# Optimization experiments

Measured on AMD Instinct MI355X. Metric: run time of the kernel, lower is better.

Reference implementation:

```python
import jax, jax.numpy as jnp
import numpy as np

EPS = 1e-20

def _conv(x, w, pad):
    return jax.lax.conv_general_dilated(
        x, w, (1, 1), [(pad, pad), (pad, pad)],
        dimension_numbers=('NCHW', 'OIHW', 'NCHW'))

def _nconv(x, c, w_raw, b, pad):
    # Normalized convolution with SoftPlus-enforced positive weights.
    w = jax.nn.softplus(w_raw)
    denom = _conv(c, w, pad)
    nomin = _conv(x * c, w, pad)
    out = nomin / (denom + EPS) + b[None, :, None, None]
    s = jnp.sum(w.reshape(w.shape[0], -1), axis=-1)  # per-out-channel kernel sum
    cout = denom / s[None, :, None, None]
    return out, cout

def _pool_gather(x, c):
    # max_pool2d(c, 2, 2, return_indices=True), then gather x at those indices.
    B, C, H, W = c.shape
    win = lambda t: t.reshape(B, C, H // 2, 2, W // 2, 2).transpose(0, 1, 2, 4, 3, 5).reshape(B, C, H // 2, W // 2, 4)
    cw, xw = win(c), win(x)
    idx = jnp.argmax(cw, axis=-1)
    take = lambda t: jnp.take_along_axis(t, idx[..., None], axis=-1)[..., 0]
    return take(xw), take(cw) / 4.0  # c1_ds /= 4

def _up2(t):
    return jnp.repeat(jnp.repeat(t, 2, axis=2), 2, axis=3)

def setup_inputs() -> dict:
    key = jax.random.key(0)
    ks = jax.random.split(key, 16)
    B, H, W, C = 8, 352, 1216, 8
    inp = {
        'x0': jax.random.normal(ks[0], (B, 1, H, W), jnp.float32),
        'c0': jax.random.uniform(ks[1], (B, 1, H, W), jnp.float32),
        'w1': jax.random.normal(ks[2], (C, 1, 5, 5), jnp.float32) * 0.1,
        'b1': jax.random.normal(ks[3], (C,), jnp.float32) * 0.01,
        'w2': jax.random.normal(ks[4], (C, C, 5, 5), jnp.float32) * 0.1,
        'b2': jax.random.normal(ks[5], (C,), jnp.float32) * 0.01,
        'w3': jax.random.normal(ks[6], (C, C, 5, 5), jnp.float32) * 0.1,
        'b3': jax.random.normal(ks[7], (C,), jnp.float32) * 0.01,
        'w4': jax.random.normal(ks[8], (C, 2 * C, 3, 3), jnp.float32) * 0.1,
        'b4': jax.random.normal(ks[9], (C,), jnp.float32) * 0.01,
        'w5': jax.random.normal(ks[10], (C, 2 * C, 3, 3), jnp.float32) * 0.1,
        'b5': jax.random.normal(ks[11], (C,), jnp.float32) * 0.01,
        'w6': jax.random.normal(ks[12], (C, 2 * C, 3, 3), jnp.float32) * 0.1,
        'b6': jax.random.normal(ks[13], (C,), jnp.float32) * 0.01,
        'w7': jax.random.normal(ks[14], (1, C, 1, 1), jnp.float32) * 0.1,
        'b7': jax.random.normal(ks[15], (1,), jnp.float32) * 0.01,
    }
    return inp

def reference(x0, c0, w1, b1, w2, b2, w3, b3, w4, b4, w5, b5, w6, b6, w7, b7):
    x1, c1 = _nconv(x0, c0, w1, b1, 2)
    x1, c1 = _nconv(x1, c1, w2, b2, 2)
    x1, c1 = _nconv(x1, c1, w3, b3, 2)
    # downsample 1 (confidence-guided unpool indices)
    x1_ds, c1_ds = _pool_gather(x1, c1)
    x2_ds, c2_ds = _nconv(x1_ds, c1_ds, w2, b2, 2)   # nconv2 reused
    x2_ds, c2_ds = _nconv(x2_ds, c2_ds, w3, b3, 2)   # nconv3 reused
    # downsample 2
    x2_dss, c2_dss = _pool_gather(x2_ds, c2_ds)
    x3_ds, c3_ds = _nconv(x2_dss, c2_dss, w2, b2, 2)
    # downsample 3
    x3_dss, c3_dss = _pool_gather(x3_ds, c3_ds)
    x4_ds, c4_ds = _nconv(x3_dss, c3_dss, w2, b2, 2)
    # decoder with nearest upsample + concat + nconv
    x4, c4 = _up2(x4_ds), _up2(c4_ds)
    x34_ds, c34_ds = _nconv(jnp.concatenate((x3_ds, x4), 1), jnp.concatenate((c3_ds, c4), 1), w4, b4, 1)
    x34, c34 = _up2(x34_ds), _up2(c34_ds)
    x23_ds, c23_ds = _nconv(jnp.concatenate((x2_ds, x34), 1), jnp.concatenate((c2_ds, c34), 1), w5, b5, 1)
    x23, c23 = _up2(x23_ds), _up2(c23_ds)
    xout, cout = _nconv(jnp.concatenate((x23, x1), 1), jnp.concatenate((c23, c1), 1), w6, b6, 1)
    xout, cout = _nconv(xout, cout, w7, b7, 0)
    return xout, cout
```

## Files before the change

### kernel.cpp

```cpp
#include <hip/hip_runtime.h>
#include <cmath>

#define EPSV 1e-20f

typedef _Float16 f16;
typedef _Float16 v8h __attribute__((ext_vector_type(8)));
typedef _Float16 h4 __attribute__((ext_vector_type(4)));
typedef float v4f __attribute__((ext_vector_type(4)));
typedef float f32x2 __attribute__((ext_vector_type(2)));

__device__ __forceinline__ float softplusf(float x) {
    return fmaxf(x, 0.f) + log1pf(expf(-fabsf(x)));
}

__device__ __forceinline__ v8h v8h_zero() {
    v8h z = {0, 0, 0, 0, 0, 0, 0, 0};
    return z;
}

__global__ void prep_scalars(const float* __restrict__ w1, const float* __restrict__ w2,
                             const float* __restrict__ w3, const float* __restrict__ w4,
                             const float* __restrict__ w5, const float* __restrict__ w6,
                             const float* __restrict__ w7, float* __restrict__ WT) {
    __shared__ float lds[1600];
    const float* srcs[7] = {w1, w2, w3, w4, w5, w6, w7};
    const int ns[7]    = {200, 1600, 1600, 1152, 1152, 1152, 8};
    const int pers[7]  = {25, 200, 200, 144, 144, 144, 8};
    const int couts[7] = {8, 8, 8, 8, 8, 8, 1};
    int t = blockIdx.x;
    const float* src = srcs[t];
    int n = ns[t];
    for (int i = threadIdx.x; i < n; i += blockDim.x) {
        float v = softplusf(src[i]);
        lds[i] = v;
        if (t == 0) WT[i] = v;
        if (t == 6) WT[256 + i] = v;
    }
    __syncthreads();
    if ((int)threadIdx.x < couts[t]) {
        float s = 0.f;
        int per = pers[t];
        for (int i = 0; i < per; ++i) s += lds[threadIdx.x * per + i];
        WT[200 + t * 8 + threadIdx.x] = s;
    }
}

__global__ void pack_enc_frag(const float* __restrict__ w2, const float* __restrict__ w3,
                              f16* __restrict__ dst2, f16* __restrict__ dst3) {
    const float* w = blockIdx.x ? w3 : w2;
    f16* dst = blockIdx.x ? dst3 : dst2;
    for (int i = threadIdx.x; i < 7 * 64 * 8; i += blockDim.x) {
        int g = i >> 9;
        int l = (i >> 3) & 63;
        int j = i & 7;
        int co = l & 15, sub = l >> 4;
        float v = 0.f;
        if (co < 8) {
            int kh = 0, kw = 0;
            bool valid = true;
            if (g < 5) { kh = g; kw = sub; }
            else if (g == 5) { kh = sub; kw = 4; }
            else { kh = 4; kw = 4; valid = (sub == 0); }
            if (valid) v = softplusf(w[((co * 8 + j) * 5 + kh) * 5 + kw]);
        }
        dst[i] = (f16)v;
    }
}

__global__ void pack_dec_frag(const float* __restrict__ w4, const float* __restrict__ w5,
                              const float* __restrict__ w6,
                              f16* __restrict__ dst4, f16* __restrict__ dst5,
                              f16* __restrict__ dst6) {
    const float* ww[3] = {w4, w5, w6};
    f16* dd[3] = {dst4, dst5, dst6};
    const float* w = ww[blockIdx.x];
    f16* dst = dd[blockIdx.x];
    for (int i = threadIdx.x; i < 6 * 64 * 8; i += blockDim.x) {
        int g = i >> 9;
        int l = (i >> 3) & 63;
        int j = i & 7;
        int co = l & 15, sub = l >> 4;
        int block = g / 3, kh = g % 3;
        float v = 0.f;
        if (co < 8 && sub < 3) {
            v = softplusf(w[((co * 16 + block * 8 + j) * 3 + kh) * 3 + sub]);
        }
        dst[i] = (f16)v;
    }
}

__device__ __forceinline__ void load_row8_f(const float* __restrict__ row, int c0, int W,
                                            float v[8]) {
    if (c0 >= 0 && c0 + 8 <= W) {
#pragma unroll
        for (int i = 0; i < 4; ++i) {
            f32x2 t = *(const f32x2*)(row + c0 + 2 * i);
            v[2 * i] = t[0];
            v[2 * i + 1] = t[1];
        }
    } else {
#pragma unroll
        for (int i = 0; i < 8; ++i) {
            int c = c0 + i;
            v[i] = (c >= 0 && c < W) ? row[c] : 0.f;
        }
    }
}

__global__ void __launch_bounds__(256) nconv_l1(
    const float* __restrict__ x0, const float* __restrict__ c0,
    const float* __restrict__ wp, const float* __restrict__ ssum,
    const float* __restrict__ bias,
    f16* __restrict__ xcout, f16* __restrict__ cout,
    int B, int H, int W) {
    __shared__ __attribute__((aligned(16))) float wl[200];
    for (int i = threadIdx.x; i < 200; i += 256) {
        int co = i & 7, r = i >> 3;
        wl[i] = wp[co * 25 + r];
    }
    __syncthreads();

    const int Wq = W >> 2;
    int idx = blockIdx.x * 256 + threadIdx.x;
    int total = B * H * Wq;
    if (idx >= total) return;
    int w0 = (idx % Wq) << 2;
    int h = (idx / Wq) % H;
    int b = idx / (Wq * H);
    const int HW = H * W;

    float den[4][8] = {}, nom[4][8] = {};
    const float* cp = c0 + (size_t)b * HW;
    const float* xp = x0 + (size_t)b * HW;

    for (int kh = 0; kh < 5; ++kh) {
        int ih = h + kh - 2;
        if (ih < 0 || ih >= H) continue;
        float cv[8], xr[8], xv[8];
        load_row8_f(cp + (size_t)ih * W, w0 - 2, W, cv);
        load_row8_f(xp + (size_t)ih * W, w0 - 2, W, xr);
#pragma unroll
        for (int i = 0; i < 8; ++i) xv[i] = xr[i] * cv[i];
        const float* wrow = &wl[kh * 5 * 8];
#pragma unroll
        for (int kw = 0; kw < 5; ++kw) {
            const float4* wq = (const float4*)&wrow[kw * 8];
            float4 wa = wq[0], wb = wq[1];
            float wv[8] = {wa.x, wa.y, wa.z, wa.w, wb.x, wb.y, wb.z, wb.w};
#pragma unroll
            for (int co = 0; co < 8; ++co)
#pragma unroll
                for (int p = 0; p < 4; ++p) {
                    den[p][co] = fmaf(wv[co], cv[p + kw], den[p][co]);
                    nom[p][co] = fmaf(wv[co], xv[p + kw], nom[p][co]);
                }
        }
    }

    float rssv[8], bbv[8];
#pragma unroll
    for (int co = 0; co < 8; ++co) {
        rssv[co] = __builtin_amdgcn_rcpf(ssum[co]);
        bbv[co] = bias[co];
    }
    unsigned pa = (unsigned)(((b * H + h) * W + w0) * 8);
#pragma unroll
    for (int p = 0; p < 4; ++p) {
        v8h xc8, c8;
#pragma unroll
        for (int co = 0; co < 8; ++co) {
            float d = den[p][co];
            float cc = d * rssv[co];
            float xo = nom[p][co] * __builtin_amdgcn_rcpf(d + EPSV) + bbv[co];
            xc8[co] = (f16)(xo * cc);
            c8[co] = (f16)cc;
        }
        *(v8h*)(xcout + pa + p * 8) = xc8;
        *(v8h*)(cout + pa + p * 8) = c8;
    }
}

__global__ void __launch_bounds__(256) pool_nhwc(
    const f16* __restrict__ xc, const f16* __restrict__ c,
    f16* __restrict__ xo, f16* __restrict__ co_,
    int B, int H, int W) {
    int H2 = H >> 1, W2 = W >> 1, Wh = W2 >> 1;
    int idx = blockIdx.x * 256 + threadIdx.x;
    int total = B * H2 * Wh;
    if (idx >= total) return;
    int wo = (idx % Wh) * 2;
    int ho = (idx / Wh) % H2;
    int b = idx / (Wh * H2);
    unsigned base = (unsigned)(((b * H + 2 * ho) * W + 2 * wo) * 8);
    unsigned rb = (unsigned)(W * 8);
    v8h c0r[4], c1r[4], x0r[4], x1r[4];
#pragma unroll
    for (int i = 0; i < 4; ++i) {
        c0r[i] = *(const v8h*)(c + base + 8 * i);
        c1r[i] = *(const v8h*)(c + base + rb + 8 * i);
        x0r[i] = *(const v8h*)(xc + base + 8 * i);
        x1r[i] = *(const v8h*)(xc + base + rb + 8 * i);
    }
    unsigned oa = (unsigned)(((b * H2 + ho) * W2 + wo) * 8);
#pragma unroll
    for (int p = 0; p < 2; ++p) {
        v8h xr, cr;
#pragma unroll
        for (int e = 0; e < 8; ++e) {
            float b0 = (float)c0r[2 * p][e], b1 = (float)c0r[2 * p + 1][e];
            float b2 = (float)c1r[2 * p][e], b3 = (float)c1r[2 * p + 1][e];
            float cb = b0;
            float xv = (float)x0r[2 * p][e];
            if (b1 > cb) { cb = b1; xv = (float)x0r[2 * p + 1][e]; }
            if (b2 > cb) { cb = b2; xv = (float)x1r[2 * p][e]; }
            if (b3 > cb) { cb = b3; xv = (float)x1r[2 * p + 1][e]; }
            xr[e] = (f16)(xv * 0.25f);
            cr[e] = (f16)(cb * 0.25f);
        }
        *(v8h*)(xo + oa + p * 8) = xr;
        *(v8h*)(co_ + oa + p * 8) = cr;
    }
}

__global__ void __launch_bounds__(256) enc5_mfma(
    const f16* __restrict__ xcin, const f16* __restrict__ cin,
    const f16* __restrict__ bfrag, const float* __restrict__ ssum,
    const float* __restrict__ bias,
    f16* __restrict__ xcout, f16* __restrict__ cout,
    int B, int H, int W, int CH) {
    const int lane = threadIdx.x & 63;
    const int wid = threadIdx.x >> 6;
    const int m = lane & 15, sub = lane >> 4;
    const int tilesW = (W + 15) >> 4;
    const int tw = blockIdx.x * 4 + wid;
    if (tw >= tilesW) return;
    const int w0 = tw << 4;
    const int b = blockIdx.z;
    const int h0 = blockIdx.y * CH;

    v8h bf[7];
#pragma unroll
    for (int g = 0; g < 7; ++g)
        bf[g] = *(const v8h*)(bfrag + ((g << 6) + lane) * 8);

    const int cwr = w0 + m + sub - 2;
    const bool okc_r = (cwr >= 0) && (cwr < W);
    const unsigned a_rot = (unsigned)min(max(cwr, 0), W - 1) * 8;
    const int cwe = w0 + m + 2;
    const bool okc_e = cwe < W;
    const unsigned a_e = (unsigned)min(cwe, W - 1) * 8;

    float4 ssv = {1.f, 1.f, 1.f, 1.f}, bbv = {0.f, 0.f, 0.f, 0.f};
    if (sub < 2) {
        ssv = *(const float4*)(ssum + sub * 4);
        bbv = *(const float4*)(bias + sub * 4);
    }
    float rssv[4];
#pragma unroll
    for (int j = 0; j < 4; ++j) rssv[j] = __builtin_amdgcn_rcpf(((const float*)&ssv)[j]);

    const unsigned W8u = (unsigned)W * 8;
    const unsigned bb8 = (unsigned)(b * H) * W8u;

    v8h Rc[5], Rx[5];
#pragma unroll
    for (int t = 0; t < 4; ++t) {
        int r = h0 - 2 + t;
        bool ok = (r >= 0) && (r < H) && okc_r;
        unsigned a = bb8 + (unsigned)min(max(r, 0), H - 1) * W8u + a_rot;
        v8h pc = *(const v8h*)(cin + a);
        v8h px = *(const v8h*)(xcin + a);
        Rc[t] = ok ? pc : v8h_zero();
        Rx[t] = ok ? px : v8h_zero();
    }
    Rc[4] = v8h_zero();
    Rx[4] = v8h_zero();

    unsigned sbase = bb8 + (unsigned)h0 * W8u + (unsigned)(w0 + m) * 8 + sub * 4;
    const bool doStore = (sub < 2) && (w0 + m < W);

    for (int hh = 0; hh < CH; hh += 5) {
#pragma unroll
        for (int p = 0; p < 5; ++p) {
            const int h = h0 + hh + p;
            {
                int r = h + 2;
                bool ok = (r < H) && okc_r;
                unsigned a = bb8 + (unsigned)min(r, H - 1) * W8u + a_rot;
                v8h pc = *(const v8h*)(cin + a);
                v8h px = *(const v8h*)(xcin + a);
                Rc[(p + 4) % 5] = ok ? pc : v8h_zero();
                Rx[(p + 4) % 5] = ok ? px : v8h_zero();
            }
            v8h e5c, e5x;
            {
                int r = h + sub - 2;
                bool ok = (r >= 0) && (r < H) && okc_e;
                unsigned a = bb8 + (unsigned)min(max(r, 0), H - 1) * W8u + a_e;
                v8h pc = *(const v8h*)(cin + a);
                v8h px = *(const v8h*)(xcin + a);
                e5c = ok ? pc : v8h_zero();
                e5x = ok ? px : v8h_zero();
            }
            v8h e6c, e6x;
            {
                int r = h + 2;
                bool ok = (r < H) && okc_e;
                unsigned a = bb8 + (unsigned)min(r, H - 1) * W8u + a_e;
                v8h pc = *(const v8h*)(cin + a);
                v8h px = *(const v8h*)(xcin + a);
                e6c = ok ? pc : v8h_zero();
                e6x = ok ? px : v8h_zero();
            }

            v4f accd = {0.f, 0.f, 0.f, 0.f}, accn = {0.f, 0.f, 0.f, 0.f};
#pragma unroll
            for (int g = 0; g < 5; ++g) {
                accd = __builtin_amdgcn_mfma_f32_16x16x32_f16(bf[g], Rc[(p + g) % 5], accd, 0, 0, 0);
                accn = __builtin_amdgcn_mfma_f32_16x16x32_f16(bf[g], Rx[(p + g) % 5], accn, 0, 0, 0);
            }
            accd = __builtin_amdgcn_mfma_f32_16x16x32_f16(bf[5], e5c, accd, 0, 0, 0);
            accn = __builtin_amdgcn_mfma_f32_16x16x32_f16(bf[5], e5x, accn, 0, 0, 0);
            accd = __builtin_amdgcn_mfma_f32_16x16x32_f16(bf[6], e6c, accd, 0, 0, 0);
            accn = __builtin_amdgcn_mfma_f32_16x16x32_f16(bf[6], e6x, accn, 0, 0, 0);

            if (doStore && h < H) {
                h4 xo8, c8;
#pragma unroll
                for (int j = 0; j < 4; ++j) {
                    float d = accd[j];
                    float cc = d * rssv[j];
                    float x = accn[j] * __builtin_amdgcn_rcpf(d + EPSV) + ((const float*)&bbv)[j];
                    c8[j] = (f16)cc;
                    xo8[j] = (f16)(x * cc);
                }
                *(h4*)(cout + sbase) = c8;
                *(h4*)(xcout + sbase) = xo8;
            }
            sbase += W8u;
        }
    }
}

template <int GR, int GS, bool FUSE7>
__global__ void __launch_bounds__(256) dec3_mfma(
    const f16* __restrict__ xcR, const f16* __restrict__ cR,
    const f16* __restrict__ xcS, const f16* __restrict__ cS,
    const f16* __restrict__ bfrag,
    const float* __restrict__ ssum, const float* __restrict__ bias,
    const float* __restrict__ wp7, const float* __restrict__ s7p,
    const float* __restrict__ b7p,
    f16* __restrict__ xcout, f16* __restrict__ ccout,
    float* __restrict__ xoutf, float* __restrict__ coutf,
    int B, int H, int W, int CH) {
    const int lane = threadIdx.x & 63;
    const int wid = threadIdx.x >> 6;
    const int m = lane & 15, sub = lane >> 4;
    const int tilesW = W >> 4;
    const int tw = blockIdx.x * 4 + wid;
    if (tw >= tilesW) return;
    const int w0 = tw << 4;
    const int b = blockIdx.z;
    const int h0 = blockIdx.y * CH;

    v8h bf[6];
#pragma unroll
    for (int g = 0; g < 6; ++g)
        bf[g] = *(const v8h*)(bfrag + ((g << 6) + lane) * 8);

    const int cw = w0 + m + sub - 1;
    const bool okc = (cw >= 0) && (cw < W);
    const int cwc = min(max(cw, 0), W - 1);
    const unsigned aR = (unsigned)cwc * 8;
    const unsigned aS = (unsigned)(cwc >> 1) * 8;

    const int Hs = H >> 1, Ws = W >> 1;
    const unsigned WR8 = (unsigned)W * 8;
    const unsigned WS8 = (unsigned)Ws * 8;
    const unsigned bbR = (unsigned)(b * H) * WR8;
    const unsigned bbS = (unsigned)(b * Hs) * WS8;

    float4 ssv = {1.f, 1.f, 1.f, 1.f}, bbv = {0.f, 0.f, 0.f, 0.f};
    float4 w7v = {0.f, 0.f, 0.f, 0.f};
    if (sub < 2) {
        ssv = *(const float4*)(ssum + sub * 4);
        bbv = *(const float4*)(bias + sub * 4);
        if (FUSE7) w7v = *(const float4*)(wp7 + sub * 4);
    }
    float rssv[4];
#pragma unroll
    for (int j = 0; j < 4; ++j) rssv[j] = __builtin_amdgcn_rcpf(((const float*)&ssv)[j]);
    float rs7 = 0.f, b7v = 0.f;
    if (FUSE7) { rs7 = __builtin_amdgcn_rcpf(s7p[0]); b7v = b7p[0]; }

    v8h Rc[3], Rx[3];
#pragma unroll
    for (int t = 0; t < 2; ++t) {
        int r = h0 - 1 + t;
        bool ok = (r >= 0) && (r < H) && okc;
        unsigned a = bbR + (unsigned)min(max(r, 0), H - 1) * WR8 + aR;
        v8h pc = *(const v8h*)(cR + a);
        v8h px = *(const v8h*)(xcR + a);
        Rc[t] = ok ? pc : v8h_zero();
        Rx[t] = ok ? px : v8h_zero();
    }
    Rc[2] = v8h_zero();
    Rx[2] = v8h_zero();

    unsigned sbase = bbR + (unsigned)h0 * WR8 + (unsigned)(w0 + m) * 8 + sub * 4;
    const bool doStore = (sub < 2);

    for (int hh = 0; hh < CH; hh += 3) {
#pragma unroll
        for (int p = 0; p < 3; ++p) {
            const int h = h0 + hh + p;
            {
                int r = h + 1;
                bool ok = (r < H) && okc;
                unsigned a = bbR + (unsigned)min(r, H - 1) * WR8 + aR;
                v8h pc = *(const v8h*)(cR + a);
                v8h px = *(const v8h*)(xcR + a);
                Rc[(p + 2) % 3] = ok ? pc : v8h_zero();
                Rx[(p + 2) % 3] = ok ? px : v8h_zero();
            }
            v8h Sc[3], Sx[3];
#pragma unroll
            for (int gs = 0; gs < 3; ++gs) {
                int r = h + gs - 1;
                bool ok = (r >= 0) && (r < H) && okc;
                unsigned a = bbS + (unsigned)(min(max(r, 0), H - 1) >> 1) * WS8 + aS;
                v8h pc = *(const v8h*)(cS + a);
                v8h px = *(const v8h*)(xcS + a);
                Sc[gs] = ok ? pc : v8h_zero();
                Sx[gs] = ok ? px : v8h_zero();
            }

            v4f accd = {0.f, 0.f, 0.f, 0.f}, accn = {0.f, 0.f, 0.f, 0.f};
#pragma unroll
            for (int g = 0; g < 3; ++g) {
                accd = __builtin_amdgcn_mfma_f32_16x16x32_f16(bf[GR + g], Rc[(p + g) % 3], accd, 0, 0, 0);
                accn = __builtin_amdgcn_mfma_f32_16x16x32_f16(bf[GR + g], Rx[(p + g) % 3], accn, 0, 0, 0);
            }
#pragma unroll
            for (int g = 0; g < 3; ++g) {
                accd = __builtin_amdgcn_mfma_f32_16x16x32_f16(bf[GS + g], Sc[g], accd, 0, 0, 0);
                accn = __builtin_amdgcn_mfma_f32_16x16x32_f16(bf[GS + g], Sx[g], accn, 0, 0, 0);
            }

            if (FUSE7) {
                if (h < H) {
                    float td = 0.f, tn = 0.f;
#pragma unroll
                    for (int j = 0; j < 4; ++j) {
                        float d = accd[j];
                        float cc = d * rssv[j];
                        float o = accn[j] * __builtin_amdgcn_rcpf(d + EPSV) + ((const float*)&bbv)[j];
                        td = fmaf(((const float*)&w7v)[j], cc, td);
                        tn = fmaf(((const float*)&w7v)[j], o * cc, tn);
                    }
                    td += __shfl_xor(td, 16);
                    tn += __shfl_xor(tn, 16);
                    td += __shfl_xor(td, 32);
                    tn += __shfl_xor(tn, 32);
                    unsigned opix = (unsigned)(b * H + h) * (unsigned)W + (unsigned)w0;
                    if (sub == 0) {
                        xoutf[opix + m] = tn * __builtin_amdgcn_rcpf(td + EPSV) + b7v;
                    } else if (sub == 1) {
                        coutf[opix + m] = td * rs7;
                    }
                }
            } else if (doStore && h < H) {
                h4 xo8, c8;
#pragma unroll
                for (int j = 0; j < 4; ++j) {
                    float d = accd[j];
                    float cc = d * rssv[j];
                    float x = accn[j] * __builtin_amdgcn_rcpf(d + EPSV) + ((const float*)&bbv)[j];
                    c8[j] = (f16)cc;
                    xo8[j] = (f16)(x * cc);
                }
                *(h4*)(ccout + sbase) = c8;
                *(h4*)(xcout + sbase) = xo8;
            }
            sbase += WR8;
        }
    }
}

extern "C" void kernel_launch(void* const* d_in, const int* in_sizes, int n_in,
                              void* d_out, int out_size, void* d_ws, size_t ws_size,
                              hipStream_t stream) {
    const float* x0 = (const float*)d_in[0];
    const float* c0 = (const float*)d_in[1];
    const float* w1 = (const float*)d_in[2];
    const float* b1 = (const float*)d_in[3];
    const float* w2 = (const float*)d_in[4];
    const float* b2 = (const float*)d_in[5];
    const float* w3 = (const float*)d_in[6];
    const float* b3 = (const float*)d_in[7];
    const float* w4 = (const float*)d_in[8];
    const float* b4 = (const float*)d_in[9];
    const float* w5 = (const float*)d_in[10];
    const float* b5 = (const float*)d_in[11];
    const float* w6 = (const float*)d_in[12];
    const float* b6 = (const float*)d_in[13];
    const float* w7 = (const float*)d_in[14];
    const float* b7 = (const float*)d_in[15];

    const int B = 8, H = 352, W = 1216;
    const int H2 = 176, W2 = 608, H4 = 88, W4 = 304, H8 = 44, W8 = 152;
    const size_t F   = (size_t)64 * H * W;
    const size_t H2s = (size_t)64 * H2 * W2;
    const size_t Qs  = (size_t)64 * H4 * W4;
    const size_t Es  = (size_t)64 * H8 * W8;

    const size_t needH = 4 * F * sizeof(f16) + 7168 * sizeof(float);
    if (ws_size < needH) return;

    f16* ws = (f16*)d_ws;
    f16* P0x = ws;
    f16* P0c = ws + F;
    f16* Ux  = ws + 2 * F;
    f16* Uc  = ws + 3 * F;
    f16* D1x = ws + 2 * F;
    f16* D1c = D1x + H2s;
    f16* D2x = D1c + H2s;
    f16* D2c = D2x + H2s;
    f16* Q1x = ws + 3 * F;
    f16* Q1c = Q1x + Qs;
    f16* Q2x = Q1c + Qs;
    f16* Q2c = Q2x + Qs;
    f16* E1x = Q2c + Qs;
    f16* E1c = E1x + Es;
    f16* E2x = E1c + Es;
    f16* E2c = E2x + Es;
    f16* DF4 = ws + 3 * F + 16777216;
    f16* DF5 = DF4 + 3072;
    f16* DF6 = DF5 + 3072;

    char* tail = (char*)d_ws + 4 * F * sizeof(f16);
    float* WT = (float*)tail;
    f16* BF2 = (f16*)(tail + 2048);
    f16* BF3 = (f16*)(tail + 9216);

    const float* s1 = WT + 200;
    const float* s2 = WT + 208;
    const float* s3 = WT + 216;
    const float* s4 = WT + 224;
    const float* s5 = WT + 232;
    const float* s6 = WT + 240;
    const float* s7 = WT + 248;
    const float* wp7 = WT + 256;

    prep_scalars<<<7, 256, 0, stream>>>(w1, w2, w3, w4, w5, w6, w7, WT);
    pack_enc_frag<<<2, 256, 0, stream>>>(w2, w3, BF2, BF3);

    auto nb = [](size_t n) { return (int)((n + 255) / 256); };
    const dim3 geF(19, 18, 8);
    const dim3 geH(10, 9, 8);
    const dim3 geQ(5, 9, 8);
    const dim3 geE(3, 9, 8);
    const dim3 gdF(19, 15, 8);
    const dim3 gdH(10, 15, 8);
    const dim3 gdQ(5, 10, 8);

    nconv_l1<<<nb((size_t)B * H * (W / 4)), 256, 0, stream>>>(
        x0, c0, WT, s1, b1, P0x, P0c, B, H, W);
    enc5_mfma<<<geF, 256, 0, stream>>>(P0x, P0c, BF2, s2, b2, Ux, Uc, B, H, W, 20);
    enc5_mfma<<<geF, 256, 0, stream>>>(Ux, Uc, BF3, s3, b3, P0x, P0c, B, H, W, 20);
    pack_dec_frag<<<3, 256, 0, stream>>>(w4, w5, w6, DF4, DF5, DF6);
    pool_nhwc<<<nb((size_t)B * H2 * (W2 / 2)), 256, 0, stream>>>(P0x, P0c, D1x, D1c, B, H, W);
    enc5_mfma<<<geH, 256, 0, stream>>>(D1x, D1c, BF2, s2, b2, D2x, D2c, B, H2, W2, 20);
    enc5_mfma<<<geH, 256, 0, stream>>>(D2x, D2c, BF3, s3, b3, D1x, D1c, B, H2, W2, 20);
    pool_nhwc<<<nb((size_t)B * H4 * (W4 / 2)), 256, 0, stream>>>(D1x, D1c, Q1x, Q1c, B, H2, W2);
    enc5_mfma<<<geQ, 256, 0, stream>>>(Q1x, Q1c, BF2, s2, b2, Q2x, Q2c, B, H4, W4, 10);
    pool_nhwc<<<nb((size_t)B * H8 * (W8 / 2)), 256, 0, stream>>>(Q2x, Q2c, E1x, E1c, B, H4, W4);
    enc5_mfma<<<geE, 256, 0, stream>>>(E1x, E1c, BF2, s2, b2, E2x, E2c, B, H8, W8, 5);

    dec3_mfma<0, 3, false><<<gdQ, 256, 0, stream>>>(
        Q2x, Q2c, E2x, E2c, DF4, s4, b4, WT, WT, WT,
        Q1x, Q1c, (float*)nullptr, (float*)nullptr, B, H4, W4, 9);
    dec3_mfma<0, 3, false><<<gdH, 256, 0, stream>>>(
        D1x, D1c, Q1x, Q1c, DF5, s5, b5, WT, WT, WT,
        D2x, D2c, (float*)nullptr, (float*)nullptr, B, H2, W2, 12);

    float* outx = (float*)d_out;
    float* outc = outx + (size_t)B * H * W;
    dec3_mfma<3, 0, true><<<gdF, 256, 0, stream>>>(
        P0x, P0c, D2x, D2c, DF6, s6, b6, wp7, s7, b7,
        (f16*)nullptr, (f16*)nullptr, outx, outc, B, H, W, 24);
}
```

Before: 421.0 us.

## Fold nearest-upsample into decoder weights and add boundary-free fast paths

The decoder weights are repacked so that taps reading the 2x nearest-upsampled skip input are pre-summed per output-row parity. Each row can then read only two low-resolution rows, loaded once per pair of output rows, instead of three upsampled rows every row. Interior tiles in both encoder and decoder kernels take a fast path without clamping and zero-select bounds checks. Grid row-chunk sizes are retuned. The cost is more code and register pressure from the duplicated paths, plus a different f16 rounding of the summed weights.

New measurement: 426.1 us. No clear change (+1.2%).

```diff
diff --git a/kernel.cpp b/kernel.cpp
--- a/kernel.cpp
+++ b/kernel.cpp
@@ -2,6 +2,7 @@
 #include <cmath>
 
 #define EPSV 1e-20f
+#define MFMA16(A, B, C) __builtin_amdgcn_mfma_f32_16x16x32_f16(A, B, C, 0, 0, 0)
 
 typedef _Float16 f16;
 typedef _Float16 v8h __attribute__((ext_vector_type(8)));
@@ -73,17 +74,26 @@
                               f16* __restrict__ dst6) {
     const float* ww[3] = {w4, w5, w6};
     f16* dd[3] = {dst4, dst5, dst6};
+    const int RBt[3] = {0, 0, 1};
     const float* w = ww[blockIdx.x];
     f16* dst = dd[blockIdx.x];
-    for (int i = threadIdx.x; i < 6 * 64 * 8; i += blockDim.x) {
+    const int rb = RBt[blockIdx.x], sbk = 1 - rb;
+    for (int i = threadIdx.x; i < 7 * 64 * 8; i += blockDim.x) {
         int g = i >> 9;
         int l = (i >> 3) & 63;
         int j = i & 7;
         int co = l & 15, sub = l >> 4;
-        int block = g / 3, kh = g % 3;
         float v = 0.f;
         if (co < 8 && sub < 3) {
-            v = softplusf(w[((co * 16 + block * 8 + j) * 3 + kh) * 3 + sub]);
+            int kw = sub;
+            auto W_ = [&](int blk, int kh) {
+                return softplusf(w[((co * 16 + blk * 8 + j) * 3 + kh) * 3 + kw]);
+            };
+            if (g < 3) v = W_(rb, g);
+            else if (g == 3) v = W_(sbk, 0);
+            else if (g == 4) v = W_(sbk, 1) + W_(sbk, 2);
+            else if (g == 5) v = W_(sbk, 0) + W_(sbk, 1);
+            else v = W_(sbk, 2);
         }
         dst[i] = (f16)v;
     }
@@ -243,13 +253,6 @@
     for (int g = 0; g < 7; ++g)
         bf[g] = *(const v8h*)(bfrag + ((g << 6) + lane) * 8);
 
-    const int cwr = w0 + m + sub - 2;
-    const bool okc_r = (cwr >= 0) && (cwr < W);
-    const unsigned a_rot = (unsigned)min(max(cwr, 0), W - 1) * 8;
-    const int cwe = w0 + m + 2;
-    const bool okc_e = cwe < W;
-    const unsigned a_e = (unsigned)min(cwe, W - 1) * 8;
-
     float4 ssv = {1.f, 1.f, 1.f, 1.f}, bbv = {0.f, 0.f, 0.f, 0.f};
     if (sub < 2) {
         ssv = *(const float4*)(ssum + sub * 4);
@@ -261,88 +264,139 @@
 
     const unsigned W8u = (unsigned)W * 8;
     const unsigned bb8 = (unsigned)(b * H) * W8u;
-
-    v8h Rc[5], Rx[5];
-#pragma unroll
-    for (int t = 0; t < 4; ++t) {
-        int r = h0 - 2 + t;
-        bool ok = (r >= 0) && (r < H) && okc_r;
-        unsigned a = bb8 + (unsigned)min(max(r, 0), H - 1) * W8u + a_rot;
-        v8h pc = *(const v8h*)(cin + a);
-        v8h px = *(const v8h*)(xcin + a);
-        Rc[t] = ok ? pc : v8h_zero();
-        Rx[t] = ok ? px : v8h_zero();
-    }
-    Rc[4] = v8h_zero();
-    Rx[4] = v8h_zero();
-
     unsigned sbase = bb8 + (unsigned)h0 * W8u + (unsigned)(w0 + m) * 8 + sub * 4;
-    const bool doStore = (sub < 2) && (w0 + m < W);
-
-    for (int hh = 0; hh < CH; hh += 5) {
-#pragma unroll
-        for (int p = 0; p < 5; ++p) {
-            const int h = h0 + hh + p;
-            {
-                int r = h + 2;
-                bool ok = (r < H) && okc_r;
-                unsigned a = bb8 + (unsigned)min(r, H - 1) * W8u + a_rot;
-                v8h pc = *(const v8h*)(cin + a);
-                v8h px = *(const v8h*)(xcin + a);
-                Rc[(p + 4) % 5] = ok ? pc : v8h_zero();
-                Rx[(p + 4) % 5] = ok ? px : v8h_zero();
-            }
-            v8h e5c, e5x;
-            {
-                int r = h + sub - 2;
-                bool ok = (r >= 0) && (r < H) && okc_e;
-                unsigned a = bb8 + (unsigned)min(max(r, 0), H - 1) * W8u + a_e;
-                v8h pc = *(const v8h*)(cin + a);
-                v8h px = *(const v8h*)(xcin + a);
-                e5c = ok ? pc : v8h_zero();
-                e5x = ok ? px : v8h_zero();
-            }
-            v8h e6c, e6x;
-            {
-                int r = h + 2;
-                bool ok = (r < H) && okc_e;
-                unsigned a = bb8 + (unsigned)min(r, H - 1) * W8u + a_e;
-                v8h pc = *(const v8h*)(cin + a);
-                v8h px = *(const v8h*)(xcin + a);
-                e6c = ok ? pc : v8h_zero();
-                e6x = ok ? px : v8h_zero();
-            }
-
-            v4f accd = {0.f, 0.f, 0.f, 0.f}, accn = {0.f, 0.f, 0.f, 0.f};
-#pragma unroll
-            for (int g = 0; g < 5; ++g) {
-                accd = __builtin_amdgcn_mfma_f32_16x16x32_f16(bf[g], Rc[(p + g) % 5], accd, 0, 0, 0);
-                accn = __builtin_amdgcn_mfma_f32_16x16x32_f16(bf[g], Rx[(p + g) % 5], accn, 0, 0, 0);
-            }
-            accd = __builtin_amdgcn_mfma_f32_16x16x32_f16(bf[5], e5c, accd, 0, 0, 0);
-            accn = __builtin_amdgcn_mfma_f32_16x16x32_f16(bf[5], e5x, accn, 0, 0, 0);
-            accd = __builtin_amdgcn_mfma_f32_16x16x32_f16(bf[6], e6c, accd, 0, 0, 0);
-            accn = __builtin_amdgcn_mfma_f32_16x16x32_f16(bf[6], e6x, accn, 0, 0, 0);
-
-            if (doStore && h < H) {
-                h4 xo8, c8;
-#pragma unroll
-                for (int j = 0; j < 4; ++j) {
-                    float d = accd[j];
-                    float cc = d * rssv[j];
-                    float x = accn[j] * __builtin_amdgcn_rcpf(d + EPSV) + ((const float*)&bbv)[j];
-                    c8[j] = (f16)cc;
-                    xo8[j] = (f16)(x * cc);
-                }
-                *(h4*)(cout + sbase) = c8;
-                *(h4*)(xcout + sbase) = xo8;
-            }
-            sbase += W8u;
-        }
-    }
-}
-
-template <int GR, int GS, bool FUSE7>
+
+    auto epi = [&](const v4f& accd, const v4f& accn, unsigned sb) {
+        h4 xo8, c8;
+#pragma unroll
+        for (int j = 0; j < 4; ++j) {
+            float d = accd[j];
+            float cc = d * rssv[j];
+            float x = accn[j] * __builtin_amdgcn_rcpf(d + EPSV) + ((const float*)&bbv)[j];
+            c8[j] = (f16)cc;
+            xo8[j] = (f16)(x * cc);
+        }
+        *(h4*)(cout + sb) = c8;
+        *(h4*)(xcout + sb) = xo8;
+    };
+
+    const bool fast = (w0 >= 2) && (w0 + 17 < W) && (h0 >= 2) && (h0 + CH + 2 <= H);
+    if (fast) {
+        v8h Rc[5], Rx[5];
+        unsigned aRot = bb8 + (unsigned)(h0 - 2) * W8u + (unsigned)(w0 + m + sub - 2) * 8;
+#pragma unroll
+        for (int t = 0; t < 4; ++t) {
+            Rc[t] = *(const v8h*)(cin + aRot);
+            Rx[t] = *(const v8h*)(xcin + aRot);
+            aRot += W8u;
+        }
+        unsigned aE5 = bb8 + (unsigned)(h0 + sub - 2) * W8u + (unsigned)(w0 + m + 2) * 8;
+        unsigned aE6 = bb8 + (unsigned)(h0 + 2) * W8u + (unsigned)(w0 + m + 2) * 8;
+        const bool st = (sub < 2);
+        for (int hh = 0; hh < CH; hh += 5) {
+#pragma unroll
+            for (int p = 0; p < 5; ++p) {
+                Rc[(p + 4) % 5] = *(const v8h*)(cin + aRot);
+                Rx[(p + 4) % 5] = *(const v8h*)(xcin + aRot);
+                aRot += W8u;
+                v8h e5c = *(const v8h*)(cin + aE5);
+                v8h e5x = *(const v8h*)(xcin + aE5);
+                aE5 += W8u;
+                v8h e6c = *(const v8h*)(cin + aE6);
+                v8h e6x = *(const v8h*)(xcin + aE6);
+                aE6 += W8u;
+
+                v4f accd = {0.f, 0.f, 0.f, 0.f}, accn = {0.f, 0.f, 0.f, 0.f};
+#pragma unroll
+                for (int g = 0; g < 5; ++g) {
+                    accd = MFMA16(bf[g], Rc[(p + g) % 5], accd);
+                    accn = MFMA16(bf[g], Rx[(p + g) % 5], accn);
+                }
+                accd = MFMA16(bf[5], e5c, accd);
+                accn = MFMA16(bf[5], e5x, accn);
+                accd = MFMA16(bf[6], e6c, accd);
+                accn = MFMA16(bf[6], e6x, accn);
+
+                if (st) epi(accd, accn, sbase);
+                sbase += W8u;
+            }
+        }
+    } else {
+        const int cwr = w0 + m + sub - 2;
+        const bool okc_r = (cwr >= 0) && (cwr < W);
+        const unsigned a_rot = (unsigned)min(max(cwr, 0), W - 1) * 8;
+        const int cwe = w0 + m + 2;
+        const bool okc_e = cwe < W;
+        const unsigned a_e = (unsigned)min(cwe, W - 1) * 8;
+        const bool doStore = (sub < 2) && (w0 + m < W);
+
+        v8h Rc[5], Rx[5];
+#pragma unroll
+        for (int t = 0; t < 4; ++t) {
+            int r = h0 - 2 + t;
+            bool ok = (r >= 0) && (r < H) && okc_r;
+            unsigned a = bb8 + (unsigned)min(max(r, 0), H - 1) * W8u + a_rot;
+            v8h pc = *(const v8h*)(cin + a);
+            v8h px = *(const v8h*)(xcin + a);
+            Rc[t] = ok ? pc : v8h_zero();
+            Rx[t] = ok ? px : v8h_zero();
+        }
+        Rc[4] = v8h_zero();
+        Rx[4] = v8h_zero();
+
+        for (int hh = 0; hh < CH; hh += 5) {
+#pragma unroll
+            for (int p = 0; p < 5; ++p) {
+                const int h = h0 + hh + p;
+                {
+                    int r = h + 2;
+                    bool ok = (r < H) && okc_r;
+                    unsigned a = bb8 + (unsigned)min(r, H - 1) * W8u + a_rot;
+                    v8h pc = *(const v8h*)(cin + a);
+                    v8h px = *(const v8h*)(xcin + a);
+                    Rc[(p + 4) % 5] = ok ? pc : v8h_zero();
+                    Rx[(p + 4) % 5] = ok ? px : v8h_zero();
+                }
+                v8h e5c, e5x;
+                {
+                    int r = h + sub - 2;
+                    bool ok = (r >= 0) && (r < H) && okc_e;
+                    unsigned a = bb8 + (unsigned)min(max(r, 0), H - 1) * W8u + a_e;
+                    v8h pc = *(const v8h*)(cin + a);
+                    v8h px = *(const v8h*)(xcin + a);
+                    e5c = ok ? pc : v8h_zero();
+                    e5x = ok ? px : v8h_zero();
+                }
+                v8h e6c, e6x;
+                {
+                    int r = h + 2;
+                    bool ok = (r < H) && okc_e;
+                    unsigned a = bb8 + (unsigned)min(r, H - 1) * W8u + a_e;
+                    v8h pc = *(const v8h*)(cin + a);
+                    v8h px = *(const v8h*)(xcin + a);
+                    e6c = ok ? pc : v8h_zero();
+                    e6x = ok ? px : v8h_zero();
+                }
+
+                v4f accd = {0.f, 0.f, 0.f, 0.f}, accn = {0.f, 0.f, 0.f, 0.f};
+#pragma unroll
+                for (int g = 0; g < 5; ++g) {
+                    accd = MFMA16(bf[g], Rc[(p + g) % 5], accd);
+                    accn = MFMA16(bf[g], Rx[(p + g) % 5], accn);
+                }
+                accd = MFMA16(bf[5], e5c, accd);
+                accn = MFMA16(bf[5], e5x, accn);
+                accd = MFMA16(bf[6], e6c, accd);
+                accn = MFMA16(bf[6], e6x, accn);
+
+                if (doStore && h < H) epi(accd, accn, sbase);
+                sbase += W8u;
+            }
+        }
+    }
+}
+
+template <bool FUSE7>
 __global__ void __launch_bounds__(256) dec3_mfma(
     const f16* __restrict__ xcR, const f16* __restrict__ cR,
     const f16* __restrict__ xcS, const f16* __restrict__ cS,
@@ -363,16 +417,16 @@
     const int b = blockIdx.z;
     const int h0 = blockIdx.y * CH;
 
-    v8h bf[6];
-#pragma unroll
-    for (int g = 0; g < 6; ++g)
+    v8h bf[7];
+#pragma unroll
+    for (int g = 0; g < 7; ++g)
         bf[g] = *(const v8h*)(bfrag + ((g << 6) + lane) * 8);
 
     const int cw = w0 + m + sub - 1;
     const bool okc = (cw >= 0) && (cw < W);
     const int cwc = min(max(cw, 0), W - 1);
-    const unsigned aR = (unsigned)cwc * 8;
-    const unsigned aS = (unsigned)(cwc >> 1) * 8;
+    const unsigned aRc = (unsigned)cwc * 8;
+    const unsigned aSc = (unsigned)(cwc >> 1) * 8;
 
     const int Hs = H >> 1, Ws = W >> 1;
     const unsigned WR8 = (unsigned)W * 8;
@@ -393,83 +447,31 @@
     float rs7 = 0.f, b7v = 0.f;
     if (FUSE7) { rs7 = __builtin_amdgcn_rcpf(s7p[0]); b7v = b7p[0]; }
 
-    v8h Rc[3], Rx[3];
-#pragma unroll
-    for (int t = 0; t < 2; ++t) {
-        int r = h0 - 1 + t;
-        bool ok = (r >= 0) && (r < H) && okc;
-        unsigned a = bbR + (unsigned)min(max(r, 0), H - 1) * WR8 + aR;
-        v8h pc = *(const v8h*)(cR + a);
-        v8h px = *(const v8h*)(xcR + a);
-        Rc[t] = ok ? pc : v8h_zero();
-        Rx[t] = ok ? px : v8h_zero();
-    }
-    Rc[2] = v8h_zero();
-    Rx[2] = v8h_zero();
-
     unsigned sbase = bbR + (unsigned)h0 * WR8 + (unsigned)(w0 + m) * 8 + sub * 4;
-    const bool doStore = (sub < 2);
-
-    for (int hh = 0; hh < CH; hh += 3) {
-#pragma unroll
-        for (int p = 0; p < 3; ++p) {
-            const int h = h0 + hh + p;
-            {
-                int r = h + 1;
-                bool ok = (r < H) && okc;
-                unsigned a = bbR + (unsigned)min(r, H - 1) * WR8 + aR;
-                v8h pc = *(const v8h*)(cR + a);
-                v8h px = *(const v8h*)(xcR + a);
-                Rc[(p + 2) % 3] = ok ? pc : v8h_zero();
-                Rx[(p + 2) % 3] = ok ? px : v8h_zero();
-            }
-            v8h Sc[3], Sx[3];
-#pragma unroll
-            for (int gs = 0; gs < 3; ++gs) {
-                int r = h + gs - 1;
-                bool ok = (r >= 0) && (r < H) && okc;
-                unsigned a = bbS + (unsigned)(min(max(r, 0), H - 1) >> 1) * WS8 + aS;
-                v8h pc = *(const v8h*)(cS + a);
-                v8h px = *(const v8h*)(xcS + a);
-                Sc[gs] = ok ? pc : v8h_zero();
-                Sx[gs] = ok ? px : v8h_zero();
-            }
-
-            v4f accd = {0.f, 0.f, 0.f, 0.f}, accn = {0.f, 0.f, 0.f, 0.f};
-#pragma unroll
-            for (int g = 0; g < 3; ++g) {
-                accd = __builtin_amdgcn_mfma_f32_16x16x32_f16(bf[GR + g], Rc[(p + g) % 3], accd, 0, 0, 0);
-                accn = __builtin_amdgcn_mfma_f32_16x16x32_f16(bf[GR + g], Rx[(p + g) % 3], accn, 0, 0, 0);
-            }
-#pragma unroll
-            for (int g = 0; g < 3; ++g) {
-                accd = __builtin_amdgcn_mfma_f32_16x16x32_f16(bf[GS + g], Sc[g], accd, 0, 0, 0);
-                accn = __builtin_amdgcn_mfma_f32_16x16x32_f16(bf[GS + g], Sx[g], accn, 0, 0, 0);
-            }
-
-            if (FUSE7) {
-                if (h < H) {
-                    float td = 0.f, tn = 0.f;
-#pragma unroll
-                    for (int j = 0; j < 4; ++j) {
-                        float d = accd[j];
-                        float cc = d * rssv[j];
-                        float o = accn[j] * __builtin_amdgcn_rcpf(d + EPSV) + ((const float*)&bbv)[j];
-                        td = fmaf(((const float*)&w7v)[j], cc, td);
-                        tn = fmaf(((const float*)&w7v)[j], o * cc, tn);
-                    }
-                    td += __shfl_xor(td, 16);
-                    tn += __shfl_xor(tn, 16);
-                    td += __shfl_xor(td, 32);
-                    tn += __shfl_xor(tn, 32);
-                    unsigned opix = (unsigned)(b * H + h) * (unsigned)W + (unsigned)w0;
-                    if (sub == 0) {
-                        xoutf[opix + m] = tn * __builtin_amdgcn_rcpf(td + EPSV) + b7v;
-                    } else if (sub == 1) {
-                        coutf[opix + m] = td * rs7;
-                    }
-                }
-            } else if (doStore && h < H) {
+    unsigned opix = (unsigned)(b * H + h0) * (unsigned)W + (unsigned)w0;
+
+    auto epi = [&](const v4f& accd, const v4f& accn) {
+        if constexpr (FUSE7) {
+            float td = 0.f, tn = 0.f;
+#pragma unroll
+            for (int j = 0; j < 4; ++j) {
+                float d = accd[j];
+                float cc = d * rssv[j];
+                float o = accn[j] * __builtin_amdgcn_rcpf(d + EPSV) + ((const float*)&bbv)[j];
+                td = fmaf(((const float*)&w7v)[j], cc, td);
+                tn = fmaf(((const float*)&w7v)[j], o * cc, tn);
+            }
+            td += __shfl_xor(td, 16);
+            tn += __shfl_xor(tn, 16);
+            td += __shfl_xor(td, 32);
+            tn += __shfl_xor(tn, 32);
+            if (sub == 0) {
+                xoutf[opix + m] = tn * __builtin_amdgcn_rcpf(td + EPSV) + b7v;
+            } else if (sub == 1) {
+                coutf[opix + m] = td * rs7;
+            }
+        } else {
+            if (sub < 2) {
                 h4 xo8, c8;
 #pragma unroll
                 for (int j = 0; j < 4; ++j) {
@@ -482,7 +484,97 @@
                 *(h4*)(ccout + sbase) = c8;
                 *(h4*)(xcout + sbase) = xo8;
             }
+        }
+    };
+
+    const bool fast = (w0 >= 1) && (w0 + 17 < W) && (h0 >= 2) && (h0 + CH + 1 <= H);
+    if (fast) {
+        v8h Rc_[3], Rx_[3], Sc_[3], Sx_[3];
+        unsigned ar = bbR + (unsigned)(h0 - 1) * WR8 + aRc;
+        Rc_[2] = *(const v8h*)(cR + ar); Rx_[2] = *(const v8h*)(xcR + ar); ar += WR8;
+        Rc_[0] = *(const v8h*)(cR + ar); Rx_[0] = *(const v8h*)(xcR + ar); ar += WR8;
+        const int k0 = h0 >> 1;
+        unsigned as_ = bbS + (unsigned)(k0 - 1) * WS8 + aSc;
+        Sc_[2] = *(const v8h*)(cS + as_); Sx_[2] = *(const v8h*)(xcS + as_); as_ += WS8;
+        Sc_[0] = *(const v8h*)(cS + as_); Sx_[0] = *(const v8h*)(xcS + as_); as_ += WS8;
+
+        for (int hh = 0; hh < CH; hh += 6) {
+#pragma unroll
+            for (int p = 0; p < 6; ++p) {
+                const int j = p >> 1;
+                Rc_[(p + 1) % 3] = *(const v8h*)(cR + ar);
+                Rx_[(p + 1) % 3] = *(const v8h*)(xcR + ar);
+                ar += WR8;
+                if ((p & 1) == 0) {
+                    Sc_[(j + 1) % 3] = *(const v8h*)(cS + as_);
+                    Sx_[(j + 1) % 3] = *(const v8h*)(xcS + as_);
+                    as_ += WS8;
+                }
+                v4f accd = {0.f, 0.f, 0.f, 0.f}, accn = {0.f, 0.f, 0.f, 0.f};
+#pragma unroll
+                for (int g = 0; g < 3; ++g) {
+                    accd = MFMA16(bf[g], Rc_[(p + g + 2) % 3], accd);
+                    accn = MFMA16(bf[g], Rx_[(p + g + 2) % 3], accn);
+                }
+                if ((p & 1) == 0) {
+                    accd = MFMA16(bf[3], Sc_[(j + 2) % 3], accd);
+                    accn = MFMA16(bf[3], Sx_[(j + 2) % 3], accn);
+                    accd = MFMA16(bf[4], Sc_[j % 3], accd);
+                    accn = MFMA16(bf[4], Sx_[j % 3], accn);
+                } else {
+                    accd = MFMA16(bf[5], Sc_[j % 3], accd);
+                    accn = MFMA16(bf[5], Sx_[j % 3], accn);
+                    accd = MFMA16(bf[6], Sc_[(j + 1) % 3], accd);
+                    accn = MFMA16(bf[6], Sx_[(j + 1) % 3], accn);
+                }
+                epi(accd, accn);
+                sbase += WR8;
+                opix += W;
+            }
+        }
+    } else {
+        for (int hh = 0; hh < CH; ++hh) {
+            const int h = h0 + hh;
+            if (h >= H) break;
+            const int k = h >> 1;
+            const bool ev = (h & 1) == 0;
+            v4f accd = {0.f, 0.f, 0.f, 0.f}, accn = {0.f, 0.f, 0.f, 0.f};
+#pragma unroll
+            for (int g = 0; g < 3; ++g) {
+                int r = h + g - 1;
+                bool ok = okc && (r >= 0) && (r < H);
+                unsigned a = bbR + (unsigned)min(max(r, 0), H - 1) * WR8 + aRc;
+                v8h pc = *(const v8h*)(cR + a);
+                v8h px = *(const v8h*)(xcR + a);
+                if (!ok) { pc = v8h_zero(); px = v8h_zero(); }
+                accd = MFMA16(bf[g], pc, accd);
+                accn = MFMA16(bf[g], px, accn);
+            }
+            {
+                int rs = ev ? (k - 1) : k;
+                bool ok = okc && (!ev || (h >= 1));
+                unsigned a = bbS + (unsigned)min(max(rs, 0), Hs - 1) * WS8 + aSc;
+                v8h pc = *(const v8h*)(cS + a);
+                v8h px = *(const v8h*)(xcS + a);
+                if (!ok) { pc = v8h_zero(); px = v8h_zero(); }
+                v8h wA = ev ? bf[3] : bf[5];
+                accd = MFMA16(wA, pc, accd);
+                accn = MFMA16(wA, px, accn);
+            }
+            {
+                int rs = ev ? k : (k + 1);
+                bool ok = okc && (ev || (h + 1 < H));
+                unsigned a = bbS + (unsigned)min(max(rs, 0), Hs - 1) * WS8 + aSc;
+                v8h pc = *(const v8h*)(cS + a);
+                v8h px = *(const v8h*)(xcS + a);
+                if (!ok) { pc = v8h_zero(); px = v8h_zero(); }
+                v8h wB = ev ? bf[4] : bf[6];
+                accd = MFMA16(wB, pc, accd);
+                accn = MFMA16(wB, px, accn);
+            }
+            epi(accd, accn);
             sbase += WR8;
+            opix += W;
         }
     }
 }
@@ -535,8 +627,8 @@
     f16* E2x = E1c + Es;
     f16* E2c = E2x + Es;
     f16* DF4 = ws + 3 * F + 16777216;
-    f16* DF5 = DF4 + 3072;
-    f16* DF6 = DF5 + 3072;
+    f16* DF5 = DF4 + 3584;
+    f16* DF6 = DF5 + 3584;
 
     char* tail = (char*)d_ws + 4 * F * sizeof(f16);
     float* WT = (float*)tail;
@@ -560,9 +652,9 @@
     const dim3 geH(10, 9, 8);
     const dim3 geQ(5, 9, 8);
     const dim3 geE(3, 9, 8);
-    const dim3 gdF(19, 15, 8);
+    const dim3 gdF(19, 30, 8);
     const dim3 gdH(10, 15, 8);
-    const dim3 gdQ(5, 10, 8);
+    const dim3 gdQ(5, 8, 8);
 
     nconv_l1<<<nb((size_t)B * H * (W / 4)), 256, 0, stream>>>(
         x0, c0, WT, s1, b1, P0x, P0c, B, H, W);
@@ -577,16 +669,16 @@
     pool_nhwc<<<nb((size_t)B * H8 * (W8 / 2)), 256, 0, stream>>>(Q2x, Q2c, E1x, E1c, B, H4, W4);
     enc5_mfma<<<geE, 256, 0, stream>>>(E1x, E1c, BF2, s2, b2, E2x, E2c, B, H8, W8, 5);
 
-    dec3_mfma<0, 3, false><<<gdQ, 256, 0, stream>>>(
+    dec3_mfma<false><<<gdQ, 256, 0, stream>>>(
         Q2x, Q2c, E2x, E2c, DF4, s4, b4, WT, WT, WT,
-        Q1x, Q1c, (float*)nullptr, (float*)nullptr, B, H4, W4, 9);
-    dec3_mfma<0, 3, false><<<gdH, 256, 0, stream>>>(
+        Q1x, Q1c, (float*)nullptr, (float*)nullptr, B, H4, W4, 12);
+    dec3_mfma<false><<<gdH, 256, 0, stream>>>(
         D1x, D1c, Q1x, Q1c, DF5, s5, b5, WT, WT, WT,
         D2x, D2c, (float*)nullptr, (float*)nullptr, B, H2, W2, 12);
 
     float* outx = (float*)d_out;
     float* outc = outx + (size_t)B * H * W;
-    dec3_mfma<3, 0, true><<<gdF, 256, 0, stream>>>(
+    dec3_mfma<true><<<gdF, 256, 0, stream>>>(
         P0x, P0c, D2x, D2c, DF6, s6, b6, wp7, s7, b7,
-        (f16*)nullptr, (f16*)nullptr, outx, outc, B, H, W, 24);
-}
+        (f16*)nullptr, (f16*)nullptr, outx, outc, B, H, W, 12);
+}
```
